# Kernel optimization log

Hardware: AMD Instinct MI355X
Metric: run time of the kernel (lower is better)

Reference implementation:

```python
import jax, jax.numpy as jnp
import numpy as np

NUM_STEPS = 20
START_IDX = 1


def setup_inputs() -> dict:
    key = jax.random.key(0)
    ks = jax.random.split(key, 14)
    B, L, D, H, E, K, V = 128, 49, 2048, 2048, 512, 512, 10000
    s = 0.02  # weight init scale to avoid saturating tanh/sigmoid
    return {
        "spatial": jax.random.normal(ks[0], (B, L, D), jnp.float32),
        "global_": jax.random.normal(ks[1], (B, D), jnp.float32),
        "embed": jax.random.normal(ks[2], (V, E), jnp.float32) * s,
        "W_ih": jax.random.normal(ks[3], (4 * H, E + D), jnp.float32) * s,
        "W_hh": jax.random.normal(ks[4], (4 * H, H), jnp.float32) * s,
        "b_ih": jnp.zeros((4 * H,), jnp.float32),
        "b_hh": jnp.zeros((4 * H,), jnp.float32),
        "W_v": jax.random.normal(ks[5], (D, K), jnp.float32) * s,
        "W_g": jax.random.normal(ks[6], (H, K), jnp.float32) * s,
        "w_h": jax.random.normal(ks[7], (K,), jnp.float32) * s,
        "W_p_w": jax.random.normal(ks[8], (V, H), jnp.float32) * s,
        "W_p_b": jnp.zeros((V,), jnp.float32),
        "W_init_h": jax.random.normal(ks[9], (D, H), jnp.float32) * s,
        "W_init_m": jax.random.normal(ks[10], (D, H), jnp.float32) * s,
    }


def reference(spatial, global_, embed, W_ih, W_hh, b_ih, b_hh,
              W_v, W_g, w_h, W_p_w, W_p_b, W_init_h, W_init_m):
    B = spatial.shape[0]
    Hdim = W_hh.shape[1]
    # initialize_state(features.global_)
    h0 = jnp.tanh(global_ @ W_init_h)
    m0 = jnp.tanh(global_ @ W_init_m)
    tok0 = jnp.full((B,), START_IDX, dtype=jnp.int32)
    # precompute attention projection of spatial features: [B, L, K]
    spatial_proj = jnp.einsum('bld,dk->blk', spatial, W_v)

    def step(carry, _):
        h, m, token = carry
        w = embed[token]                                  # [B, E]
        x = jnp.concatenate([w, global_], axis=1)         # [B, E+D]
        gates = x @ W_ih.T + b_ih + h @ W_hh.T + b_hh     # [B, 4H]
        i_g, f_g, g_g, o_g = jnp.split(gates, 4, axis=1)  # torch gate order
        m_new = jax.nn.sigmoid(f_g) * m + jax.nn.sigmoid(i_g) * jnp.tanh(g_g)
        h_new = jax.nn.sigmoid(o_g) * jnp.tanh(m_new)
        # spatial attention: z = w_h^T tanh(W_v V + W_g h)
        z = jnp.tanh(spatial_proj + (h_new @ W_g)[:, None, :]) @ w_h  # [B, L]
        alpha = jax.nn.softmax(z, axis=1)
        c = jnp.einsum('bl,bld->bd', alpha, spatial)      # [B, D]
        logits = (c + h_new) @ W_p_w.T + W_p_b            # [B, V]
        token_new = jnp.argmax(logits, axis=1).astype(jnp.int32)
        return (h_new, m_new, token_new), (logits, token_new)

    _, (logits_seq, tokens) = jax.lax.scan(step, (h0, m0, tok0), None, length=NUM_STEPS)
    # [T, B, V] -> [B, T, V]; [T, B] -> [B, T]
    return jnp.transpose(logits_seq, (1, 0, 2)), tokens.T
```

## Files before the change

kernel.cpp:

```cpp
#include <hip/hip_runtime.h>
#include <math.h>


typedef __attribute__((ext_vector_type(8))) short bf16x8;
typedef __attribute__((ext_vector_type(4))) float f32x4;

#define B_ 128
#define L_ 49
#define D_ 2048
#define H_ 2048
#define E_ 512
#define KA_ 512
#define V_ 10000
#define T_ 20
#define ED_ 2560
#define KT_ 4608
#define KT2_ 2560
#define H4_ 8192
#define VP_ 10112

__device__ __forceinline__ void split1(float x, short* hi, short* lo){
  unsigned u = __float_as_uint(x);
  *hi = (short)(u >> 16);
  float r = x - __uint_as_float(u & 0xffff0000u);
  *lo = (short)(__float_as_uint(r) >> 16);
}
__device__ __forceinline__ void split8(float4 a, float4 b, bf16x8& h, bf16x8& l){
  float xs[8] = {a.x,a.y,a.z,a.w,b.x,b.y,b.z,b.w};
#pragma unroll
  for (int i=0;i<8;++i){
    unsigned u = __float_as_uint(xs[i]);
    h[i] = (short)(u>>16);
    float r = xs[i] - __uint_as_float(u & 0xffff0000u);
    l[i] = (short)(__float_as_uint(r)>>16);
  }
}

#define MFMA16(d,a,b,c) d = __builtin_amdgcn_mfma_f32_16x16x32_bf16(a,b,c,0,0,0)

__device__ __forceinline__ void gl_lds16(const short* g, char* l){
  __builtin_amdgcn_global_load_lds(
      (const __attribute__((address_space(1))) unsigned int*)g,
      (__attribute__((address_space(3))) unsigned int*)l, 16, 0, 0);
}

__global__ __launch_bounds__(256)
void gemm_db(const short* __restrict__ A1h, const short* __restrict__ A1l, int lda1,
             const short* __restrict__ A2h, const short* __restrict__ A2l, int lda2,
             int ksplit,
             const short* __restrict__ Wh, const short* __restrict__ Wl, int ldw,
             float* __restrict__ Cp, int Mtot, int Np, int k_len)
{
  __shared__ __align__(16) char smem[131072];
  const int tid = threadIdx.x;
  const int wid = tid >> 6, lane = tid & 63;
  const int lr = lane & 15, lg = lane >> 4;
  const int m0 = blockIdx.z * 128;
  const int nblk = blockIdx.x * 128;
  const int kb0 = blockIdx.y * k_len;

  const int li8 = lane >> 3;
  const int kx  = 8 * ((lane & 7) ^ li8);

  f32x4 acc[8][2];
#pragma unroll
  for (int i=0;i<8;++i)
#pragma unroll
    for (int r=0;r<4;++r){ acc[i][0][r]=0.f; acc[i][1][r]=0.f; }

  const int rA = wid*32 + lr, rB = rA + 16;
  const int sw7 = lr & 7;

  auto STAGE = [&](int kb, int buf) {
    char* s = smem + buf*65536;
    if (wid == 0) {
#pragma unroll
      for (int j = 0; j < 16; ++j)
        gl_lds16(Wh + (long)(nblk + j*8 + li8)*ldw + kb + kx, s + j*1024);
    } else if (wid == 1) {
#pragma unroll
      for (int j = 0; j < 16; ++j)
        gl_lds16(Wl + (long)(nblk + j*8 + li8)*ldw + kb + kx, s + 16384 + j*1024);
    } else {
      const short *Ph, *Pl; int ldx, kc;
      if (kb < ksplit) { Ph = A1h; Pl = A1l; ldx = lda1; kc = kb; }
      else             { Ph = A2h; Pl = A2l; ldx = lda2; kc = kb - ksplit; }
      if (wid == 2) {
#pragma unroll
        for (int j = 0; j < 16; ++j)
          gl_lds16(Ph + (long)(m0 + j*8 + li8)*ldx + kc + kx, s + 32768 + j*1024);
      } else {
#pragma unroll
        for (int j = 0; j < 16; ++j)
          gl_lds16(Pl + (long)(m0 + j*8 + li8)*ldx + kc + kx, s + 49152 + j*1024);
      }
    }
  };

  auto COMPUTE = [&](int buf) {
    char* s = smem + buf*65536;
#pragma unroll
    for (int h = 0; h < 2; ++h) {
      const int c16 = (h<<2) + lg;
      const int swz = (c16 ^ sw7) << 4;
      const bf16x8 whA = *(const bf16x8*)(s +         rA*128 + swz);
      const bf16x8 wlA = *(const bf16x8*)(s + 16384 + rA*128 + swz);
      const bf16x8 whB = *(const bf16x8*)(s +         rB*128 + swz);
      const bf16x8 wlB = *(const bf16x8*)(s + 16384 + rB*128 + swz);
#pragma unroll
      for (int mt = 0; mt < 8; ++mt) {
        const int aoff = (mt*16 + lr)*128 + swz;
        const bf16x8 ah = *(const bf16x8*)(s + 32768 + aoff);
        const bf16x8 al = *(const bf16x8*)(s + 49152 + aoff);
        MFMA16(acc[mt][0], ah, whA, acc[mt][0]);
        MFMA16(acc[mt][1], ah, whB, acc[mt][1]);
        MFMA16(acc[mt][0], ah, wlA, acc[mt][0]);
        MFMA16(acc[mt][1], ah, wlB, acc[mt][1]);
        MFMA16(acc[mt][0], al, whA, acc[mt][0]);
        MFMA16(acc[mt][1], al, whB, acc[mt][1]);
      }
    }
  };

  STAGE(kb0, 0);
  asm volatile("s_waitcnt vmcnt(0)");
  __syncthreads();
  int cur = 0;
  for (int kt = 64; kt < k_len; kt += 64) {
    STAGE(kb0 + kt, cur ^ 1);
    COMPUTE(cur);
    asm volatile("s_waitcnt vmcnt(0)");
    __syncthreads();
    cur ^= 1;
  }
  COMPUTE(cur);

  const long srow = (long)blockIdx.y * Mtot + m0;
#pragma unroll
  for (int mt=0; mt<8; ++mt)
#pragma unroll
    for (int nt=0; nt<2; ++nt){
      const int col = nblk + wid*32 + nt*16 + lr;
#pragma unroll
      for (int r=0; r<4; ++r)
        Cp[(srow + mt*16 + 4*lg + r)*Np + col] = acc[mt][nt][r];
    }
}

__global__ __launch_bounds__(256)
void gemm_lds(const short* __restrict__ Ah, const short* __restrict__ Al, int lda,
              const short* __restrict__ Wh, const short* __restrict__ Wl, int ldw,
              float* __restrict__ Cp, int Mtot, int Np, int k_len)
{
  __shared__ __align__(16) char smem[65536];
  const int tid = threadIdx.x;
  const int wid = tid >> 6, lane = tid & 63;
  const int lr = lane & 15, lg = lane >> 4;
  const int m0 = blockIdx.z * 128;
  const int nblk = blockIdx.x * 128;
  const int kb0 = blockIdx.y * k_len;

  const int li8 = lane >> 3;
  const int kx  = 8 * ((lane & 7) ^ li8);

  f32x4 acc[8][2];
#pragma unroll
  for (int i=0;i<8;++i)
#pragma unroll
    for (int r=0;r<4;++r){ acc[i][0][r]=0.f; acc[i][1][r]=0.f; }

  const int rA = wid*32 + lr, rB = rA + 16;
  const int sw7 = lr & 7;

  for (int kt = 0; kt < k_len; kt += 64) {
    const int kb = kb0 + kt;
    if (wid == 0) {
#pragma unroll
      for (int j = 0; j < 16; ++j)
        gl_lds16(Wh + (long)(nblk + j*8 + li8)*ldw + kb + kx, smem + j*1024);
    } else if (wid == 1) {
#pragma unroll
      for (int j = 0; j < 16; ++j)
        gl_lds16(Wl + (long)(nblk + j*8 + li8)*ldw + kb + kx, smem + 16384 + j*1024);
    } else if (wid == 2) {
#pragma unroll
      for (int j = 0; j < 16; ++j)
        gl_lds16(Ah + (long)(m0 + j*8 + li8)*lda + kb + kx, smem + 32768 + j*1024);
    } else {
#pragma unroll
      for (int j = 0; j < 16; ++j)
        gl_lds16(Al + (long)(m0 + j*8 + li8)*lda + kb + kx, smem + 49152 + j*1024);
    }
    asm volatile("s_waitcnt vmcnt(0)");
    __syncthreads();

#pragma unroll
    for (int h = 0; h < 2; ++h) {
      const int c16 = (h<<2) + lg;
      const int swz = (c16 ^ sw7) << 4;
      const bf16x8 whA = *(const bf16x8*)(smem +         rA*128 + swz);
      const bf16x8 wlA = *(const bf16x8*)(smem + 16384 + rA*128 + swz);
      const bf16x8 whB = *(const bf16x8*)(smem +         rB*128 + swz);
      const bf16x8 wlB = *(const bf16x8*)(smem + 16384 + rB*128 + swz);
#pragma unroll
      for (int mt = 0; mt < 8; ++mt) {
        const int aoff = (mt*16 + lr)*128 + swz;
        const bf16x8 ah = *(const bf16x8*)(smem + 32768 + aoff);
        const bf16x8 al = *(const bf16x8*)(smem + 49152 + aoff);
        MFMA16(acc[mt][0], ah, whA, acc[mt][0]);
        MFMA16(acc[mt][1], ah, whB, acc[mt][1]);
        MFMA16(acc[mt][0], ah, wlA, acc[mt][0]);
        MFMA16(acc[mt][1], ah, wlB, acc[mt][1]);
        MFMA16(acc[mt][0], al, whA, acc[mt][0]);
        MFMA16(acc[mt][1], al, whB, acc[mt][1]);
      }
    }
    __syncthreads();
  }

  const long srow = (long)blockIdx.y * Mtot + m0;
#pragma unroll
  for (int mt=0; mt<8; ++mt)
#pragma unroll
    for (int nt=0; nt<2; ++nt){
      const int col = nblk + wid*32 + nt*16 + lr;
#pragma unroll
      for (int r=0; r<4; ++r)
        Cp[(srow + mt*16 + 4*lg + r)*Np + col] = acc[mt][nt][r];
    }
}

template<bool AF32>
__global__ __launch_bounds__(256)
void gemm_mfma(const void* Ahv, const void* Alv, int lda,
               const float* __restrict__ W1, int ldw1,
               const float* __restrict__ W2, int ldw2, int ksplit,
               float* __restrict__ Cp, int Mtot, int Np, int Nvalid, int k_len)
{
  const int tid = threadIdx.x;
  const int wid = tid >> 6, lane = tid & 63;
  const int lr = lane & 15, lg = lane >> 4;
  const int m0 = blockIdx.z * 128;
  const int nw = blockIdx.x * 128 + wid * 32;
  const int kb = blockIdx.y * k_len;

  int rowA = nw + lr;       if (rowA >= Nvalid) rowA = Nvalid - 1;
  int rowB = nw + 16 + lr;  if (rowB >= Nvalid) rowB = Nvalid - 1;

  f32x4 acc[8][2];
#pragma unroll
  for (int i=0;i<8;++i)
#pragma unroll
    for (int r=0;r<4;++r){ acc[i][0][r]=0.f; acc[i][1][r]=0.f; }

  for (int kk = 0; kk < k_len; kk += 32) {
    const int kg = kb + kk;
    const float *pA, *pB;
    if (W2 && kg >= ksplit) {
      pA = W2 + (long)rowA*ldw2 + (kg - ksplit) + 8*lg;
      pB = W2 + (long)rowB*ldw2 + (kg - ksplit) + 8*lg;
    } else {
      pA = W1 + (long)rowA*ldw1 + kg + 8*lg;
      pB = W1 + (long)rowB*ldw1 + kg + 8*lg;
    }
    bf16x8 whA, wlA, whB, wlB;
    split8(*(const float4*)pA, *(const float4*)(pA+4), whA, wlA);
    split8(*(const float4*)pB, *(const float4*)(pB+4), whB, wlB);

    bf16x8 ah[8], al[8];
    if constexpr (AF32) {
      const float* Af = (const float*)Ahv;
#pragma unroll
      for (int mt=0; mt<8; ++mt){
        const float* ap = Af + (long)(m0 + mt*16 + lr)*lda + kg + 8*lg;
        split8(*(const float4*)ap, *(const float4*)(ap+4), ah[mt], al[mt]);
      }
    } else {
      const short* Ah = (const short*)Ahv;
      const short* Al = (const short*)Alv;
#pragma unroll
      for (int mt=0; mt<8; ++mt){
        const long off = (long)(m0 + mt*16 + lr)*lda + kg + 8*lg;
        ah[mt] = *(const bf16x8*)(Ah + off);
        al[mt] = *(const bf16x8*)(Al + off);
      }
    }
#pragma unroll
    for (int mt=0; mt<8; ++mt){
      MFMA16(acc[mt][0], ah[mt], whA, acc[mt][0]);
      MFMA16(acc[mt][1], ah[mt], whB, acc[mt][1]);
      MFMA16(acc[mt][0], ah[mt], wlA, acc[mt][0]);
      MFMA16(acc[mt][1], ah[mt], wlB, acc[mt][1]);
      MFMA16(acc[mt][0], al[mt], whA, acc[mt][0]);
      MFMA16(acc[mt][1], al[mt], whB, acc[mt][1]);
    }
  }

  const long srow = (long)blockIdx.y * Mtot + m0;
#pragma unroll
  for (int mt=0; mt<8; ++mt)
#pragma unroll
// ... 218 lines not shown
    float e = (lane < L_) ? expf(v - mx) : 0.f;
    float sum = e;
#pragma unroll
    for (int off = 32; off > 0; off >>= 1) sum += __shfl_xor(sum, off);
    if (lane < L_) alph[lane] = e / sum;
  }
  __syncthreads();
  const int d4 = dh * 256 + tid;
  const float4* sp4 = (const float4*)spatial;
  float4 acc = ((const float4*)h)[(long)b * 512 + d4];
#pragma unroll 7
  for (int l = 0; l < L_; ++l) {
    const float w = alph[l];
    const float4 v = sp4[((long)b * L_ + l) * 512 + d4];
    acc.x = fmaf(w, v.x, acc.x); acc.y = fmaf(w, v.y, acc.y);
    acc.z = fmaf(w, v.z, acc.z); acc.w = fmaf(w, v.w, acc.w);
  }
  short4 hv, lv;
  split1(acc.x, &hv.x, &lv.x); split1(acc.y, &hv.y, &lv.y);
  split1(acc.z, &hv.z, &lv.z); split1(acc.w, &hv.w, &lv.w);
  *(short4*)&a_hi[(long)b * D_ + d4*4] = hv;
  *(short4*)&a_lo[(long)b * D_ + d4*4] = lv;
}

template<int SHG>
__global__ __launch_bounds__(256)
void attn_k(const float* __restrict__ sp_proj, const float* __restrict__ hgp,
            const float* __restrict__ w_h, const float* __restrict__ spatial,
            const float* __restrict__ h,
            short* __restrict__ a_hi, short* __restrict__ a_lo)
{
  const int b = blockIdx.x, half = blockIdx.y, tid = threadIdx.x;
  const int lane = tid & 63, wv = tid >> 6;
  __shared__ float hgs[KA_];
  __shared__ float whs[KA_];
  __shared__ float zs[L_];
  __shared__ float alph[L_];
  for (int i = tid; i < KA_; i += 256) {
    float s = 0.f;
#pragma unroll
    for (int sl = 0; sl < SHG; ++sl) s += hgp[((long)sl * B_ + b) * KA_ + i];
    hgs[i] = s; whs[i] = w_h[i];
  }
  __syncthreads();
  for (int l = wv; l < L_; l += 4) {
    const float* sp = sp_proj + ((long)b * L_ + l) * KA_;
    float s = 0.f;
    for (int k = lane; k < KA_; k += 64) s += whs[k] * tanhf(sp[k] + hgs[k]);
#pragma unroll
    for (int off = 32; off > 0; off >>= 1) s += __shfl_down(s, off);
    if (lane == 0) zs[l] = s;
  }
  __syncthreads();
  if (wv == 0) {
    float v = (lane < L_) ? zs[lane] : -INFINITY;
    float mx = v;
#pragma unroll
    for (int off = 32; off > 0; off >>= 1) mx = fmaxf(mx, __shfl_xor(mx, off));
    float e = (lane < L_) ? expf(v - mx) : 0.f;
    float sum = e;
#pragma unroll
    for (int off = 32; off > 0; off >>= 1) sum += __shfl_xor(sum, off);
    if (lane < L_) alph[lane] = e / sum;
  }
  __syncthreads();
  const int d4 = half * 256 + tid;
  const float4* h4 = (const float4*)h;
  const float4* sp4 = (const float4*)spatial;
  float4 acc = h4[(long)b * 512 + d4];
#pragma unroll 7
  for (int l = 0; l < L_; ++l) {
    const float w = alph[l];
    const float4 v = sp4[((long)b * L_ + l) * 512 + d4];
    acc.x = fmaf(w, v.x, acc.x); acc.y = fmaf(w, v.y, acc.y);
    acc.z = fmaf(w, v.z, acc.z); acc.w = fmaf(w, v.w, acc.w);
  }
  short4 hv, lv;
  split1(acc.x, &hv.x, &lv.x); split1(acc.y, &hv.y, &lv.y);
  split1(acc.z, &hv.z, &lv.z); split1(acc.w, &hv.w, &lv.w);
  *(short4*)&a_hi[(long)b * D_ + d4*4] = hv;
  *(short4*)&a_lo[(long)b * D_ + d4*4] = lv;
}

template<int S, bool GATHER>
__global__ __launch_bounds__(256)
void logits_argmax_k(const float* __restrict__ lp, const float* __restrict__ bias,
                     float* __restrict__ outL, int* __restrict__ tok,
                     float* __restrict__ tokout,
                     const float* __restrict__ embed,
                     short* __restrict__ xe_hi, short* __restrict__ xe_lo)
{
  const int b = blockIdx.x, tid = threadIdx.x;
  float bv = -INFINITY; int bi = 0x7fffffff;
  for (int j = tid; j < V_; j += 256) {
    float v = bias[j];
#pragma unroll
    for (int sl = 0; sl < S; ++sl) v += lp[((long)sl * B_ + b) * VP_ + j];
    outL[(long)b * (T_*V_) + j] = v;
    if (v > bv) { bv = v; bi = j; }
  }
  __shared__ float sv[256];
  __shared__ int   si[256];
  sv[tid] = bv; si[tid] = bi;
  __syncthreads();
  for (int s = 128; s > 0; s >>= 1) {
    if (tid < s) {
      const float ov = sv[tid + s]; const int oi = si[tid + s];
      if (ov > sv[tid] || (ov == sv[tid] && oi < si[tid])) { sv[tid] = ov; si[tid] = oi; }
    }
    __syncthreads();
  }
  if (tid == 0) { tok[b] = si[0]; tokout[(long)b * T_] = (float)si[0]; }
  if (GATHER) {
    __syncthreads();
    const int tk = si[0];
    const float* e = embed + (long)tk * E_;
    for (int i = tid; i < E_; i += 256)
      split1(e[i], &xe_hi[(long)b*E_ + i], &xe_lo[(long)b*E_ + i]);
  }
}

extern "C" void kernel_launch(void* const* d_in, const int* in_sizes, int n_in,
                              void* d_out, int out_size, void* d_ws, size_t ws_size,
                              hipStream_t stream)
{
  const float* spatial  = (const float*)d_in[0];
  const float* global_  = (const float*)d_in[1];
  const float* embed    = (const float*)d_in[2];
  const float* W_ih     = (const float*)d_in[3];
  const float* W_hh     = (const float*)d_in[4];
  const float* b_ih     = (const float*)d_in[5];
  const float* b_hh     = (const float*)d_in[6];
  const float* W_v      = (const float*)d_in[7];
  const float* W_g      = (const float*)d_in[8];
  const float* w_h      = (const float*)d_in[9];
  const float* W_p_w    = (const float*)d_in[10];
  const float* W_p_b    = (const float*)d_in[11];
  const float* W_init_h = (const float*)d_in[12];
  const float* W_init_m = (const float*)d_in[13];
  float* out = (float*)d_out;
  float* tokout = out + (long)B_ * T_ * V_;

  char* base = (char*)d_ws;
  const size_t NEED_PRE = 284983808;
  const size_t NEED_FB  = 62390784;
  if (ws_size < NEED_FB) return;

  if (ws_size >= NEED_PRE) {
    float* sp      = (float*)(base + 0);
    float* h       = (float*)(base + 12845056);
    float* m       = (float*)(base + 13893632);
    short* h_hi    = (short*)(base + 14942208);
    short* h_lo    = (short*)(base + 15466496);
    short* a_hi    = (short*)(base + 15990784);
    short* a_lo    = (short*)(base + 16515072);
    short* xe_hi   = (short*)(base + 17039360);
    short* xe_lo   = (short*)(base + 17170432);
    short* g_hi    = (short*)(base + 18350080);
    short* g_lo    = (short*)(base + 18874368);
    float* gconst  = (float*)(base + 19398656);
    int*   tok     = (int*)  (base + 23592960);
    float* arena   = (float*)(base + 23593472);
    short* Wcat_hi = (short*)(base + 107479552);
    short* Wcat_lo = (short*)(base + 149422592);
    short* Wp_hi   = (short*)(base + 191365632);
    short* Wp_lo   = (short*)(base + 232784384);
    short* WvT_hi  = (short*)(base + 274203136);
    short* WvT_lo  = (short*)(base + 276300288);
    short* WgT_hi  = (short*)(base + 278397440);
    short* WgT_lo  = (short*)(base + 280494592);
    float* zbuf    = (float*)(base + 282853888);

    init_tok_k<<<1, 128, 0, stream>>>(tok);
    split_plane_k<<<256, 256, 0, stream>>>(global_, (long)B_*D_, g_hi, g_lo);

    split_t_k<<<dim3(KA_/64, D_/64), 256, 0, stream>>>(W_v, D_, KA_, WvT_hi, WvT_lo);
    short* spA_hi = Wp_hi;
    short* spA_lo = (short*)((char*)Wp_hi + 25690112);
    split_plane_k<<<12544, 256, 0, stream>>>(spatial, (long)B_*L_*D_, spA_hi, spA_lo);
    float* sppart = (float*)Wcat_hi;
    gemm_db<<<dim3(4, 2, 49), 256, 0, stream>>>(
        spA_hi, spA_lo, D_, spA_hi, spA_lo, D_, 1<<30,
        WvT_hi, WvT_lo, D_, sppart, B_*L_, KA_, 1024);
    reduce_sp_k<2><<<3136, 256, 0, stream>>>((const float4*)sppart, (float4*)sp);

    short* Wglob_hi = Wp_hi;
    short* Wglob_lo = (short*)((char*)Wp_hi + 33554432);
    split_nt_k<<<dim3(2, H4_), 256, 0, stream>>>(W_ih + 512, ED_, H4_, D_, Wglob_hi, Wglob_lo, D_, 0);
    gemm_db<<<dim3(64, 4, 1), 256, 0, stream>>>(
        g_hi, g_lo, D_, g_hi, g_lo, D_, 1<<30,
        Wglob_hi, Wglob_lo, D_, arena, B_, H4_, 512);
    gred_k<4><<<(B_*H4_)/256, 256, 0, stream>>>(arena, b_ih, b_hh, gconst);

    split_nt_k<<<dim3(1, H4_), 256, 0, stream>>>(W_ih, ED_, H4_, E_, Wcat_hi, Wcat_lo, KT2_, 0);
    split_nt_k<<<dim3(2, H4_), 256, 0, stream>>>(W_hh, H_, H4_, H_, Wcat_hi, Wcat_lo, KT2_, E_);
    split_nt_k<<<dim3(2, VP_), 256, 0, stream>>>(W_p_w, H_, V_, H_, Wp_hi, Wp_lo, H_, 0);
    split_t_k<<<dim3(KA_/64, H_/64), 256, 0, stream>>>(W_g, H_, KA_, WgT_hi, WgT_lo);

    {
      short* WTh = (short*)arena;
      short* WTl = (short*)((char*)arena + 8388608);
      float* prt = (float*)((char*)arena + 16777216);
      split_t_k<<<dim3(H_/64, D_/64), 256, 0, stream>>>(W_init_h, D_, H_, WTh, WTl);
      gemm_lds<<<dim3(16, 16, 1), 256, 0, stream>>>(
          g_hi, g_lo, D_, WTh, WTl, D_, prt, B_, H_, 128);
      reduce_tanh_k<<<(B_*H_)/256, 256, 0, stream>>>(prt, 16, h, h_hi, h_lo);
      split_t_k<<<dim3(H_/64, D_/64), 256, 0, stream>>>(W_init_m, D_, H_, WTh, WTl);
      gemm_lds<<<dim3(16, 16, 1), 256, 0, stream>>>(
          g_hi, g_lo, D_, WTh, WTl, D_, prt, B_, H_, 128);
      reduce_tanh_k<<<(B_*H_)/256, 256, 0, stream>>>(prt, 16, m, nullptr, nullptr);
    }

    gather_emb_k<<<B_, 256, 0, stream>>>(embed, tok, xe_hi, xe_lo);

    for (int t = 0; t < T_; ++t) {
      gemm_db<<<dim3(64, 4, 1), 256, 0, stream>>>(
          xe_hi, xe_lo, E_, h_hi, h_lo, H_, E_,
          Wcat_hi, Wcat_lo, KT2_, arena, B_, H4_, 640);
      lstm_reduce_k<4><<<(B_*H_)/256, 256, 0, stream>>>(
          arena, gconst, nullptr, nullptr, h, m, h_hi, h_lo);
      gemm_lds<<<dim3(4, 32, 1), 256, 0, stream>>>(
          h_hi, h_lo, H_, WgT_hi, WgT_lo, H_, arena, B_, KA_, 64);
      hgz_k<<<B_, 256, 0, stream>>>(arena, sp, w_h, zbuf);
      cfull_k<<<dim3(B_, 2), 256, 0, stream>>>(zbuf, spatial, h, a_hi, a_lo);
      gemm_db<<<dim3(79, 4, 1), 256, 0, stream>>>(
          a_hi, a_lo, H_, a_hi, a_lo, H_, 1<<30,
          Wp_hi, Wp_lo, H_, arena, B_, VP_, 512);
      logits_argmax_k<4,true><<<B_, 256, 0, stream>>>(
          arena, W_p_b, out + (long)t * V_, tok, tokout + t,
          embed, xe_hi, xe_lo);
    }
  } else {
    float* sp    = (float*)(base + 0);
    float* WvTf  = (float*)(base + 12845056);
    float* WgTf  = (float*)(base + 17039360);
    float* h     = (float*)(base + 21233664);
    float* m     = (float*)(base + 22282240);
    short* h_hi  = (short*)(base + 24379392);
    short* h_lo  = (short*)(base + 24903680);
    short* a_hi  = (short*)(base + 25427968);
    short* a_lo  = (short*)(base + 25952256);
    short* xh_hi = (short*)(base + 26476544);
    short* xh_lo = (short*)(base + 27656192);
    int*   tok   = (int*)  (base + 28835840);
    float* arena = (float*)(base + 28836352);

    init_tok_k<<<1, 128, 0, stream>>>(tok);
    transpose_f32<<<dim3(KA_/64, D_/64), 256, 0, stream>>>(W_v, D_, KA_, WvTf);
    gemm_mfma<true><<<dim3(4, 1, 49), 256, 0, stream>>>(
        spatial, nullptr, D_, WvTf, D_, nullptr, 0, 1<<30, sp, B_*L_, KA_, KA_, D_);
    transpose_f32<<<dim3(KA_/64, H_/64), 256, 0, stream>>>(W_g, H_, KA_, WgTf);
    {
      float* WT  = arena;
      float* prt = (float*)((char*)arena + 16777216);
      transpose_f32<<<dim3(H_/64, D_/64), 256, 0, stream>>>(W_init_h, D_, H_, WT);
      gemm_mfma<true><<<dim3(16, 4, 1), 256, 0, stream>>>(
          global_, nullptr, D_, WT, D_, nullptr, 0, 1<<30, prt, B_, H_, H_, 512);
      reduce_tanh_k<<<(B_*H_)/256, 256, 0, stream>>>(prt, 4, h, h_hi, h_lo);
      transpose_f32<<<dim3(H_/64, D_/64), 256, 0, stream>>>(W_init_m, D_, H_, WT);
      gemm_mfma<true><<<dim3(16, 4, 1), 256, 0, stream>>>(
          global_, nullptr, D_, WT, D_, nullptr, 0, 1<<30, prt, B_, H_, H_, 512);
      reduce_tanh_k<<<(B_*H_)/256, 256, 0, stream>>>(prt, 4, m, nullptr, nullptr);
    }
    for (int t = 0; t < T_; ++t) {
      gather_xh_k<<<B_, 256, 0, stream>>>(embed, global_, h_hi, h_lo, tok, xh_hi, xh_lo);
      gemm_mfma<false><<<dim3(64, 8, 1), 256, 0, stream>>>(
          xh_hi, xh_lo, KT_, W_ih, ED_, W_hh, H_, ED_, arena, B_, H4_, H4_, 576);
      lstm_reduce_k<8><<<(B_*H_)/256, 256, 0, stream>>>(
          arena, nullptr, b_ih, b_hh, h, m, h_hi, h_lo);
      gemm_mfma<false><<<dim3(4, 16, 1), 256, 0, stream>>>(
          h_hi, h_lo, H_, WgTf, H_, nullptr, 0, 1<<30, arena, B_, KA_, KA_, 128);
      attn_k<16><<<dim3(B_, 2), 256, 0, stream>>>(sp, arena, w_h, spatial, h, a_hi, a_lo);
      gemm_mfma<false><<<dim3(79, 4, 1), 256, 0, stream>>>(
          a_hi, a_lo, H_, W_p_w, H_, nullptr, 0, 1<<30, arena, B_, VP_, V_, 512);
      logits_argmax_k<4,false><<<B_, 256, 0, stream>>>(
          arena, W_p_b, out + (long)t * V_, tok, tokout + t,
          nullptr, nullptr, nullptr);
    }
  }
}
```

Before: 2.762 ms.

## Unify GEMMs into one kernel staging one operand in LDS, other in registers

Replaces the two GEMM kernels with a templated kernel that double-buffers only one operand (weights or activations) in LDS while the other operand is loaded directly from global into registers. LDS use is halved so two blocks can fit per CU (launch_bounds 256,2), and split-K factors are doubled across the recurrent and setup GEMMs, with the partial-sum reduction kernels widened to match. This aims to raise occupancy and parallelism for the small-M LSTM-step GEMMs, at the cost of more register pressure, uncoalesced direct global loads, and more partial-sum traffic to reduce.

```diff
diff --git a/kernel.cpp b/kernel.cpp
--- a/kernel.cpp
+++ b/kernel.cpp
@@ -44,111 +44,11 @@
       (__attribute__((address_space(3))) unsigned int*)l, 16, 0, 0);
 }
 
-__global__ __launch_bounds__(256)
-void gemm_db(const short* __restrict__ A1h, const short* __restrict__ A1l, int lda1,
-             const short* __restrict__ A2h, const short* __restrict__ A2l, int lda2,
-             int ksplit,
-             const short* __restrict__ Wh, const short* __restrict__ Wl, int ldw,
-             float* __restrict__ Cp, int Mtot, int Np, int k_len)
-{
-  __shared__ __align__(16) char smem[131072];
-  const int tid = threadIdx.x;
-  const int wid = tid >> 6, lane = tid & 63;
-  const int lr = lane & 15, lg = lane >> 4;
-  const int m0 = blockIdx.z * 128;
-  const int nblk = blockIdx.x * 128;
-  const int kb0 = blockIdx.y * k_len;
-
-  const int li8 = lane >> 3;
-  const int kx  = 8 * ((lane & 7) ^ li8);
-
-  f32x4 acc[8][2];
-#pragma unroll
-  for (int i=0;i<8;++i)
-#pragma unroll
-    for (int r=0;r<4;++r){ acc[i][0][r]=0.f; acc[i][1][r]=0.f; }
-
-  const int rA = wid*32 + lr, rB = rA + 16;
-  const int sw7 = lr & 7;
-
-  auto STAGE = [&](int kb, int buf) {
-    char* s = smem + buf*65536;
-    if (wid == 0) {
-#pragma unroll
-      for (int j = 0; j < 16; ++j)
-        gl_lds16(Wh + (long)(nblk + j*8 + li8)*ldw + kb + kx, s + j*1024);
-    } else if (wid == 1) {
-#pragma unroll
-      for (int j = 0; j < 16; ++j)
-        gl_lds16(Wl + (long)(nblk + j*8 + li8)*ldw + kb + kx, s + 16384 + j*1024);
-    } else {
-      const short *Ph, *Pl; int ldx, kc;
-      if (kb < ksplit) { Ph = A1h; Pl = A1l; ldx = lda1; kc = kb; }
-      else             { Ph = A2h; Pl = A2l; ldx = lda2; kc = kb - ksplit; }
-      if (wid == 2) {
-#pragma unroll
-        for (int j = 0; j < 16; ++j)
-          gl_lds16(Ph + (long)(m0 + j*8 + li8)*ldx + kc + kx, s + 32768 + j*1024);
-      } else {
-#pragma unroll
-        for (int j = 0; j < 16; ++j)
-          gl_lds16(Pl + (long)(m0 + j*8 + li8)*ldx + kc + kx, s + 49152 + j*1024);
-      }
-    }
-  };
-
-  auto COMPUTE = [&](int buf) {
-    char* s = smem + buf*65536;
-#pragma unroll
-    for (int h = 0; h < 2; ++h) {
-      const int c16 = (h<<2) + lg;
-      const int swz = (c16 ^ sw7) << 4;
-      const bf16x8 whA = *(const bf16x8*)(s +         rA*128 + swz);
-      const bf16x8 wlA = *(const bf16x8*)(s + 16384 + rA*128 + swz);
-      const bf16x8 whB = *(const bf16x8*)(s +         rB*128 + swz);
-      const bf16x8 wlB = *(const bf16x8*)(s + 16384 + rB*128 + swz);
-#pragma unroll
-      for (int mt = 0; mt < 8; ++mt) {
-        const int aoff = (mt*16 + lr)*128 + swz;
-        const bf16x8 ah = *(const bf16x8*)(s + 32768 + aoff);
-        const bf16x8 al = *(const bf16x8*)(s + 49152 + aoff);
-        MFMA16(acc[mt][0], ah, whA, acc[mt][0]);
-        MFMA16(acc[mt][1], ah, whB, acc[mt][1]);
-        MFMA16(acc[mt][0], ah, wlA, acc[mt][0]);
-        MFMA16(acc[mt][1], ah, wlB, acc[mt][1]);
-        MFMA16(acc[mt][0], al, whA, acc[mt][0]);
-        MFMA16(acc[mt][1], al, whB, acc[mt][1]);
-      }
-    }
-  };
-
-  STAGE(kb0, 0);
-  asm volatile("s_waitcnt vmcnt(0)");
-  __syncthreads();
-  int cur = 0;
-  for (int kt = 64; kt < k_len; kt += 64) {
-    STAGE(kb0 + kt, cur ^ 1);
-    COMPUTE(cur);
-    asm volatile("s_waitcnt vmcnt(0)");
-    __syncthreads();
-    cur ^= 1;
-  }
-  COMPUTE(cur);
-
-  const long srow = (long)blockIdx.y * Mtot + m0;
-#pragma unroll
-  for (int mt=0; mt<8; ++mt)
-#pragma unroll
-    for (int nt=0; nt<2; ++nt){
-      const int col = nblk + wid*32 + nt*16 + lr;
-#pragma unroll
-      for (int r=0; r<4; ++r)
-        Cp[(srow + mt*16 + 4*lg + r)*Np + col] = acc[mt][nt][r];
-    }
-}
-
-__global__ __launch_bounds__(256)
-void gemm_lds(const short* __restrict__ Ah, const short* __restrict__ Al, int lda,
+template<bool STAGE_A>
+__global__ __launch_bounds__(256, 2)
+void gemm_v10(const short* __restrict__ A1h, const short* __restrict__ A1l, int lda1,
+              const short* __restrict__ A2h, const short* __restrict__ A2l, int lda2,
+              int ksplit,
               const short* __restrict__ Wh, const short* __restrict__ Wl, int ldw,
               float* __restrict__ Cp, int Mtot, int Np, int k_len)
 {
@@ -159,9 +59,10 @@
   const int m0 = blockIdx.z * 128;
   const int nblk = blockIdx.x * 128;
   const int kb0 = blockIdx.y * k_len;
-
   const int li8 = lane >> 3;
   const int kx  = 8 * ((lane & 7) ^ li8);
+  const int r0s = (wid & 1) * 64;
+  char* const splane = smem + (wid >> 1) * 16384;
 
   f32x4 acc[8][2];
 #pragma unroll
@@ -169,53 +70,110 @@
 #pragma unroll
     for (int r=0;r<4;++r){ acc[i][0][r]=0.f; acc[i][1][r]=0.f; }
 
-  const int rA = wid*32 + lr, rB = rA + 16;
+  const int rL = wid*32 + lr, rLB = rL + 16;
+  const long rWA = (long)(nblk + wid*32 + lr);
+  const long rWB = rWA + 16;
   const int sw7 = lr & 7;
 
+  auto STAGE = [&](int kb, int buf) {
+    char* s = splane + buf*32768;
+    if constexpr (STAGE_A) {
+      const short* P = (wid >= 2) ? A1l : A1h;
+#pragma unroll
+      for (int j = 0; j < 8; ++j)
+        gl_lds16(P + (long)(m0 + r0s + j*8 + li8)*lda1 + kb + kx, s + (r0s + j*8)*128);
+    } else {
+      const short* P = (wid >= 2) ? Wl : Wh;
+#pragma unroll
+      for (int j = 0; j < 8; ++j)
+        gl_lds16(P + (long)(nblk + r0s + j*8 + li8)*ldw + kb + kx, s + (r0s + j*8)*128);
+    }
+  };
+
+  STAGE(kb0, 0);
+  asm volatile("s_waitcnt vmcnt(0)");
+  __syncthreads();
+  int cur = 0;
+
   for (int kt = 0; kt < k_len; kt += 64) {
-    const int kb = kb0 + kt;
-    if (wid == 0) {
-#pragma unroll
-      for (int j = 0; j < 16; ++j)
-        gl_lds16(Wh + (long)(nblk + j*8 + li8)*ldw + kb + kx, smem + j*1024);
-    } else if (wid == 1) {
-#pragma unroll
-      for (int j = 0; j < 16; ++j)
-        gl_lds16(Wl + (long)(nblk + j*8 + li8)*ldw + kb + kx, smem + 16384 + j*1024);
-    } else if (wid == 2) {
-#pragma unroll
-      for (int j = 0; j < 16; ++j)
-        gl_lds16(Ah + (long)(m0 + j*8 + li8)*lda + kb + kx, smem + 32768 + j*1024);
+    const int kbb = kb0 + kt;
+    const bool last = (kt + 64 >= k_len);
+    char* s = smem + cur*32768;
+
+    if constexpr (STAGE_A) {
+      bf16x8 w0hA, w0lA, w0hB, w0lB, w1hA, w1lA, w1hB, w1lB;
+      {
+        const long c0 = kbb + 8*lg;
+        w0hA = *(const bf16x8*)(Wh + rWA*ldw + c0);
+        w0lA = *(const bf16x8*)(Wl + rWA*ldw + c0);
+        w0hB = *(const bf16x8*)(Wh + rWB*ldw + c0);
+        w0lB = *(const bf16x8*)(Wl + rWB*ldw + c0);
+        w1hA = *(const bf16x8*)(Wh + rWA*ldw + c0 + 32);
+        w1lA = *(const bf16x8*)(Wl + rWA*ldw + c0 + 32);
+        w1hB = *(const bf16x8*)(Wh + rWB*ldw + c0 + 32);
+        w1lB = *(const bf16x8*)(Wl + rWB*ldw + c0 + 32);
+      }
+      if (!last) STAGE(kbb + 64, cur ^ 1);
+#pragma unroll
+      for (int h = 0; h < 2; ++h) {
+        const int swz = ((h*4 + lg) ^ sw7) << 4;
+        const bf16x8 whA = h ? w1hA : w0hA;
+        const bf16x8 wlA = h ? w1lA : w0lA;
+        const bf16x8 whB = h ? w1hB : w0hB;
+        const bf16x8 wlB = h ? w1lB : w0lB;
+#pragma unroll
+        for (int mt = 0; mt < 8; ++mt) {
+          const int aoff = (mt*16 + lr)*128 + swz;
+          const bf16x8 ah = *(const bf16x8*)(s + aoff);
+          const bf16x8 al = *(const bf16x8*)(s + 16384 + aoff);
+          MFMA16(acc[mt][0], ah, whA, acc[mt][0]);
+          MFMA16(acc[mt][1], ah, whB, acc[mt][1]);
+          MFMA16(acc[mt][0], ah, wlA, acc[mt][0]);
+          MFMA16(acc[mt][1], ah, wlB, acc[mt][1]);
+          MFMA16(acc[mt][0], al, whA, acc[mt][0]);
+          MFMA16(acc[mt][1], al, whB, acc[mt][1]);
+        }
+      }
     } else {
-#pragma unroll
-      for (int j = 0; j < 16; ++j)
-        gl_lds16(Al + (long)(m0 + j*8 + li8)*lda + kb + kx, smem + 49152 + j*1024);
+      bf16x8 a0h[8], a0l[8], a1h[8], a1l[8];
+#pragma unroll
+      for (int h = 0; h < 2; ++h) {
+        const int kg = kbb + h*32;
+        const short *Ph, *Pl; long co; int ldx;
+        if (kg < ksplit) { Ph = A1h; Pl = A1l; co = kg; ldx = lda1; }
+        else             { Ph = A2h; Pl = A2l; co = kg - ksplit; ldx = lda2; }
+        co += 8*lg;
+#pragma unroll
+        for (int mt = 0; mt < 8; ++mt) {
+          const long o = (long)(m0 + mt*16 + lr)*ldx + co;
+          if (h == 0) { a0h[mt] = *(const bf16x8*)(Ph + o); a0l[mt] = *(const bf16x8*)(Pl + o); }
+          else        { a1h[mt] = *(const bf16x8*)(Ph + o); a1l[mt] = *(const bf16x8*)(Pl + o); }
+        }
+      }
+      if (!last) STAGE(kbb + 64, cur ^ 1);
+#pragma unroll
+      for (int h = 0; h < 2; ++h) {
+        const int swz = ((h*4 + lg) ^ sw7) << 4;
+        const bf16x8 whA = *(const bf16x8*)(s +         rL*128 + swz);
+        const bf16x8 wlA = *(const bf16x8*)(s + 16384 + rL*128 + swz);
+        const bf16x8 whB = *(const bf16x8*)(s +         rLB*128 + swz);
+        const bf16x8 wlB = *(const bf16x8*)(s + 16384 + rLB*128 + swz);
+#pragma unroll
+        for (int mt = 0; mt < 8; ++mt) {
+          const bf16x8 ah = h ? a1h[mt] : a0h[mt];
+          const bf16x8 al = h ? a1l[mt] : a0l[mt];
+          MFMA16(acc[mt][0], ah, whA, acc[mt][0]);
+          MFMA16(acc[mt][1], ah, whB, acc[mt][1]);
+          MFMA16(acc[mt][0], ah, wlA, acc[mt][0]);
+          MFMA16(acc[mt][1], ah, wlB, acc[mt][1]);
+          MFMA16(acc[mt][0], al, whA, acc[mt][0]);
+          MFMA16(acc[mt][1], al, whB, acc[mt][1]);
+        }
+      }
     }
     asm volatile("s_waitcnt vmcnt(0)");
     __syncthreads();
-
-#pragma unroll
-    for (int h = 0; h < 2; ++h) {
-      const int c16 = (h<<2) + lg;
-      const int swz = (c16 ^ sw7) << 4;
-      const bf16x8 whA = *(const bf16x8*)(smem +         rA*128 + swz);
-      const bf16x8 wlA = *(const bf16x8*)(smem + 16384 + rA*128 + swz);
-      const bf16x8 whB = *(const bf16x8*)(smem +         rB*128 + swz);
-      const bf16x8 wlB = *(const bf16x8*)(smem + 16384 + rB*128 + swz);
-#pragma unroll
-      for (int mt = 0; mt < 8; ++mt) {
-        const int aoff = (mt*16 + lr)*128 + swz;
-        const bf16x8 ah = *(const bf16x8*)(smem + 32768 + aoff);
-        const bf16x8 al = *(const bf16x8*)(smem + 49152 + aoff);
-        MFMA16(acc[mt][0], ah, whA, acc[mt][0]);
-        MFMA16(acc[mt][1], ah, whB, acc[mt][1]);
-        MFMA16(acc[mt][0], ah, wlA, acc[mt][0]);
-        MFMA16(acc[mt][1], ah, wlB, acc[mt][1]);
-        MFMA16(acc[mt][0], al, whA, acc[mt][0]);
-        MFMA16(acc[mt][1], al, whB, acc[mt][1]);
-      }
-    }
-    __syncthreads();
+    cur ^= 1;
   }
 
   const long srow = (long)blockIdx.y * Mtot + m0;
@@ -698,18 +656,18 @@
     short* spA_lo = (short*)((char*)Wp_hi + 25690112);
     split_plane_k<<<12544, 256, 0, stream>>>(spatial, (long)B_*L_*D_, spA_hi, spA_lo);
     float* sppart = (float*)Wcat_hi;
-    gemm_db<<<dim3(4, 2, 49), 256, 0, stream>>>(
+    gemm_v10<true><<<dim3(4, 4, 49), 256, 0, stream>>>(
         spA_hi, spA_lo, D_, spA_hi, spA_lo, D_, 1<<30,
-        WvT_hi, WvT_lo, D_, sppart, B_*L_, KA_, 1024);
-    reduce_sp_k<2><<<3136, 256, 0, stream>>>((const float4*)sppart, (float4*)sp);
+        WvT_hi, WvT_lo, D_, sppart, B_*L_, KA_, 512);
+    reduce_sp_k<4><<<3136, 256, 0, stream>>>((const float4*)sppart, (float4*)sp);
 
     short* Wglob_hi = Wp_hi;
     short* Wglob_lo = (short*)((char*)Wp_hi + 33554432);
     split_nt_k<<<dim3(2, H4_), 256, 0, stream>>>(W_ih + 512, ED_, H4_, D_, Wglob_hi, Wglob_lo, D_, 0);
-    gemm_db<<<dim3(64, 4, 1), 256, 0, stream>>>(
+    gemm_v10<false><<<dim3(64, 8, 1), 256, 0, stream>>>(
         g_hi, g_lo, D_, g_hi, g_lo, D_, 1<<30,
-        Wglob_hi, Wglob_lo, D_, arena, B_, H4_, 512);
-    gred_k<4><<<(B_*H4_)/256, 256, 0, stream>>>(arena, b_ih, b_hh, gconst);
+        Wglob_hi, Wglob_lo, D_, arena, B_, H4_, 256);
+    gred_k<8><<<(B_*H4_)/256, 256, 0, stream>>>(arena, b_ih, b_hh, gconst);
 
     split_nt_k<<<dim3(1, H4_), 256, 0, stream>>>(W_ih, ED_, H4_, E_, Wcat_hi, Wcat_lo, KT2_, 0);
     split_nt_k<<<dim3(2, H4_), 256, 0, stream>>>(W_hh, H_, H4_, H_, Wcat_hi, Wcat_lo, KT2_, E_);
@@ -721,31 +679,34 @@
       short* WTl = (short*)((char*)arena + 8388608);
       float* prt = (float*)((char*)arena + 16777216);
       split_t_k<<<dim3(H_/64, D_/64), 256, 0, stream>>>(W_init_h, D_, H_, WTh, WTl);
-      gemm_lds<<<dim3(16, 16, 1), 256, 0, stream>>>(
-          g_hi, g_lo, D_, WTh, WTl, D_, prt, B_, H_, 128);
+      gemm_v10<false><<<dim3(16, 16, 1), 256, 0, stream>>>(
+          g_hi, g_lo, D_, g_hi, g_lo, D_, 1<<30,
+          WTh, WTl, D_, prt, B_, H_, 128);
       reduce_tanh_k<<<(B_*H_)/256, 256, 0, stream>>>(prt, 16, h, h_hi, h_lo);
       split_t_k<<<dim3(H_/64, D_/64), 256, 0, stream>>>(W_init_m, D_, H_, WTh, WTl);
-      gemm_lds<<<dim3(16, 16, 1), 256, 0, stream>>>(
-          g_hi, g_lo, D_, WTh, WTl, D_, prt, B_, H_, 128);
+      gemm_v10<false><<<dim3(16, 16, 1), 256, 0, stream>>>(
+          g_hi, g_lo, D_, g_hi, g_lo, D_, 1<<30,
+          WTh, WTl, D_, prt, B_, H_, 128);
       reduce_tanh_k<<<(B_*H_)/256, 256, 0, stream>>>(prt, 16, m, nullptr, nullptr);
     }
 
     gather_emb_k<<<B_, 256, 0, stream>>>(embed, tok, xe_hi, xe_lo);
 
     for (int t = 0; t < T_; ++t) {
-      gemm_db<<<dim3(64, 4, 1), 256, 0, stream>>>(
+      gemm_v10<false><<<dim3(64, 8, 1), 256, 0, stream>>>(
           xe_hi, xe_lo, E_, h_hi, h_lo, H_, E_,
-          Wcat_hi, Wcat_lo, KT2_, arena, B_, H4_, 640);
-      lstm_reduce_k<4><<<(B_*H_)/256, 256, 0, stream>>>(
+          Wcat_hi, Wcat_lo, KT2_, arena, B_, H4_, 320);
+      lstm_reduce_k<8><<<(B_*H_)/256, 256, 0, stream>>>(
           arena, gconst, nullptr, nullptr, h, m, h_hi, h_lo);
-      gemm_lds<<<dim3(4, 32, 1), 256, 0, stream>>>(
-          h_hi, h_lo, H_, WgT_hi, WgT_lo, H_, arena, B_, KA_, 64);
+      gemm_v10<false><<<dim3(4, 32, 1), 256, 0, stream>>>(
+          h_hi, h_lo, H_, h_hi, h_lo, H_, 1<<30,
+          WgT_hi, WgT_lo, H_, arena, B_, KA_, 64);
       hgz_k<<<B_, 256, 0, stream>>>(arena, sp, w_h, zbuf);
       cfull_k<<<dim3(B_, 2), 256, 0, stream>>>(zbuf, spatial, h, a_hi, a_lo);
-      gemm_db<<<dim3(79, 4, 1), 256, 0, stream>>>(
+      gemm_v10<false><<<dim3(79, 8, 1), 256, 0, stream>>>(
           a_hi, a_lo, H_, a_hi, a_lo, H_, 1<<30,
-          Wp_hi, Wp_lo, H_, arena, B_, VP_, 512);
-      logits_argmax_k<4,true><<<B_, 256, 0, stream>>>(
+          Wp_hi, Wp_lo, H_, arena, B_, VP_, 256);
+      logits_argmax_k<8,true><<<B_, 256, 0, stream>>>(
           arena, W_p_b, out + (long)t * V_, tok, tokout + t,
           embed, xe_hi, xe_lo);
     }
```

New measurement: 4.441 ms. 1.61x slower.

## Swap double-buffered GEMMs for wider split-K LDS GEMM and split logits argmax

Applied to the files above, without the earlier changes.

The per-step LSTM-gate and vocabulary-projection GEMMs move from the double-buffered gemm_db kernel to a single-buffered gemm_lds kernel, which gains support for two A operands. The split-K factor doubles from 4 to 8, giving twice as many workgroups and halving each block's K range. The logits reduce plus argmax is split into a vocab-partitioned kernel across 8 blocks per row and a small finalize kernel that also gathers the next embedding. The aim is more parallelism for these small-batch GEMMs and the reduction, at the cost of more partial-sum traffic, an extra launch per step, and losing load/compute overlap.

```diff
diff --git a/kernel.cpp b/kernel.cpp
--- a/kernel.cpp
+++ b/kernel.cpp
@@ -45,6 +45,96 @@
 }
 
 __global__ __launch_bounds__(256)
+void gemm_lds(const short* __restrict__ A1h, const short* __restrict__ A1l, int lda1,
+              const short* __restrict__ A2h, const short* __restrict__ A2l, int lda2,
+              int ksplit,
+              const short* __restrict__ Wh, const short* __restrict__ Wl, int ldw,
+              float* __restrict__ Cp, int Mtot, int Np, int k_len)
+{
+  __shared__ __align__(16) char smem[65536];
+  const int tid = threadIdx.x;
+  const int wid = tid >> 6, lane = tid & 63;
+  const int lr = lane & 15, lg = lane >> 4;
+  const int m0 = blockIdx.z * 128;
+  const int nblk = blockIdx.x * 128;
+  const int kb0 = blockIdx.y * k_len;
+
+  const int li8 = lane >> 3;
+  const int kx  = 8 * ((lane & 7) ^ li8);
+
+  f32x4 acc[8][2];
+#pragma unroll
+  for (int i=0;i<8;++i)
+#pragma unroll
+    for (int r=0;r<4;++r){ acc[i][0][r]=0.f; acc[i][1][r]=0.f; }
+
+  const int rA = wid*32 + lr, rB = rA + 16;
+  const int sw7 = lr & 7;
+
+  for (int kt = 0; kt < k_len; kt += 64) {
+    const int kb = kb0 + kt;
+    if (wid == 0) {
+#pragma unroll
+      for (int j = 0; j < 16; ++j)
+        gl_lds16(Wh + (long)(nblk + j*8 + li8)*ldw + kb + kx, smem + j*1024);
+    } else if (wid == 1) {
+#pragma unroll
+      for (int j = 0; j < 16; ++j)
+        gl_lds16(Wl + (long)(nblk + j*8 + li8)*ldw + kb + kx, smem + 16384 + j*1024);
+    } else {
+      const short *Ph, *Pl; int ldx, kc;
+      if (kb < ksplit) { Ph = A1h; Pl = A1l; ldx = lda1; kc = kb; }
+      else             { Ph = A2h; Pl = A2l; ldx = lda2; kc = kb - ksplit; }
+      if (wid == 2) {
+#pragma unroll
+        for (int j = 0; j < 16; ++j)
+          gl_lds16(Ph + (long)(m0 + j*8 + li8)*ldx + kc + kx, smem + 32768 + j*1024);
+      } else {
+#pragma unroll
+        for (int j = 0; j < 16; ++j)
+          gl_lds16(Pl + (long)(m0 + j*8 + li8)*ldx + kc + kx, smem + 49152 + j*1024);
+      }
+    }
+    asm volatile("s_waitcnt vmcnt(0)");
+    __syncthreads();
+
+#pragma unroll
+    for (int h = 0; h < 2; ++h) {
+      const int c16 = (h<<2) + lg;
+      const int swz = (c16 ^ sw7) << 4;
+      const bf16x8 whA = *(const bf16x8*)(smem +         rA*128 + swz);
+      const bf16x8 wlA = *(const bf16x8*)(smem + 16384 + rA*128 + swz);
+      const bf16x8 whB = *(const bf16x8*)(smem +         rB*128 + swz);
+      const bf16x8 wlB = *(const bf16x8*)(smem + 16384 + rB*128 + swz);
+#pragma unroll
+      for (int mt = 0; mt < 8; ++mt) {
+        const int aoff = (mt*16 + lr)*128 + swz;
+        const bf16x8 ah = *(const bf16x8*)(smem + 32768 + aoff);
+        const bf16x8 al = *(const bf16x8*)(smem + 49152 + aoff);
+        MFMA16(acc[mt][0], ah, whA, acc[mt][0]);
+        MFMA16(acc[mt][1], ah, whB, acc[mt][1]);
+        MFMA16(acc[mt][0], ah, wlA, acc[mt][0]);
+        MFMA16(acc[mt][1], ah, wlB, acc[mt][1]);
+        MFMA16(acc[mt][0], al, whA, acc[mt][0]);
+        MFMA16(acc[mt][1], al, whB, acc[mt][1]);
+      }
+    }
+    __syncthreads();
+  }
+
+  const long srow = (long)blockIdx.y * Mtot + m0;
+#pragma unroll
+  for (int mt=0; mt<8; ++mt)
+#pragma unroll
+    for (int nt=0; nt<2; ++nt){
+      const int col = nblk + wid*32 + nt*16 + lr;
+#pragma unroll
+      for (int r=0; r<4; ++r)
+        Cp[(srow + mt*16 + 4*lg + r)*Np + col] = acc[mt][nt][r];
+    }
+}
+
+__global__ __launch_bounds__(256)
 void gemm_db(const short* __restrict__ A1h, const short* __restrict__ A1l, int lda1,
              const short* __restrict__ A2h, const short* __restrict__ A2l, int lda2,
              int ksplit,
@@ -134,89 +224,6 @@
     cur ^= 1;
   }
   COMPUTE(cur);
-
-  const long srow = (long)blockIdx.y * Mtot + m0;
-#pragma unroll
-  for (int mt=0; mt<8; ++mt)
-#pragma unroll
-    for (int nt=0; nt<2; ++nt){
-      const int col = nblk + wid*32 + nt*16 + lr;
-#pragma unroll
-      for (int r=0; r<4; ++r)
-        Cp[(srow + mt*16 + 4*lg + r)*Np + col] = acc[mt][nt][r];
-    }
-}
-
-__global__ __launch_bounds__(256)
-void gemm_lds(const short* __restrict__ Ah, const short* __restrict__ Al, int lda,
-              const short* __restrict__ Wh, const short* __restrict__ Wl, int ldw,
-              float* __restrict__ Cp, int Mtot, int Np, int k_len)
-{
-  __shared__ __align__(16) char smem[65536];
-  const int tid = threadIdx.x;
-  const int wid = tid >> 6, lane = tid & 63;
-  const int lr = lane & 15, lg = lane >> 4;
-  const int m0 = blockIdx.z * 128;
-  const int nblk = blockIdx.x * 128;
-  const int kb0 = blockIdx.y * k_len;
-
-  const int li8 = lane >> 3;
-  const int kx  = 8 * ((lane & 7) ^ li8);
-
-  f32x4 acc[8][2];
-#pragma unroll
-  for (int i=0;i<8;++i)
-#pragma unroll
-    for (int r=0;r<4;++r){ acc[i][0][r]=0.f; acc[i][1][r]=0.f; }
-
-  const int rA = wid*32 + lr, rB = rA + 16;
-  const int sw7 = lr & 7;
-
-  for (int kt = 0; kt < k_len; kt += 64) {
-    const int kb = kb0 + kt;
-    if (wid == 0) {
-#pragma unroll
-      for (int j = 0; j < 16; ++j)
-        gl_lds16(Wh + (long)(nblk + j*8 + li8)*ldw + kb + kx, smem + j*1024);
-    } else if (wid == 1) {
-#pragma unroll
-      for (int j = 0; j < 16; ++j)
-        gl_lds16(Wl + (long)(nblk + j*8 + li8)*ldw + kb + kx, smem + 16384 + j*1024);
-    } else if (wid == 2) {
-#pragma unroll
-      for (int j = 0; j < 16; ++j)
-        gl_lds16(Ah + (long)(m0 + j*8 + li8)*lda + kb + kx, smem + 32768 + j*1024);
-    } else {
-#pragma unroll
-      for (int j = 0; j < 16; ++j)
-        gl_lds16(Al + (long)(m0 + j*8 + li8)*lda + kb + kx, smem + 49152 + j*1024);
-    }
-    asm volatile("s_waitcnt vmcnt(0)");
-    __syncthreads();
-
-#pragma unroll
-    for (int h = 0; h < 2; ++h) {
-      const int c16 = (h<<2) + lg;
-      const int swz = (c16 ^ sw7) << 4;
-      const bf16x8 whA = *(const bf16x8*)(smem +         rA*128 + swz);
-      const bf16x8 wlA = *(const bf16x8*)(smem + 16384 + rA*128 + swz);
-      const bf16x8 whB = *(const bf16x8*)(smem +         rB*128 + swz);
-      const bf16x8 wlB = *(const bf16x8*)(smem + 16384 + rB*128 + swz);
-#pragma unroll
-      for (int mt = 0; mt < 8; ++mt) {
-        const int aoff = (mt*16 + lr)*128 + swz;
-        const bf16x8 ah = *(const bf16x8*)(smem + 32768 + aoff);
-        const bf16x8 al = *(const bf16x8*)(smem + 49152 + aoff);
-        MFMA16(acc[mt][0], ah, whA, acc[mt][0]);
-        MFMA16(acc[mt][1], ah, whB, acc[mt][1]);
-        MFMA16(acc[mt][0], ah, wlA, acc[mt][0]);
-        MFMA16(acc[mt][1], ah, wlB, acc[mt][1]);
-        MFMA16(acc[mt][0], al, whA, acc[mt][0]);
-        MFMA16(acc[mt][1], al, whB, acc[mt][1]);
-      }
-    }
-    __syncthreads();
-  }
 
   const long srow = (long)blockIdx.y * Mtot + m0;
 #pragma unroll
@@ -601,13 +608,66 @@
   *(short4*)&a_lo[(long)b * D_ + d4*4] = lv;
 }
 
-template<int S, bool GATHER>
+template<int S>
+__global__ __launch_bounds__(256)
+void logits_part_k(const float* __restrict__ lp, const float* __restrict__ bias,
+                   float* __restrict__ outL, float* __restrict__ cval,
+                   int* __restrict__ cidx)
+{
+  const int b = blockIdx.x, s8 = blockIdx.y, tid = threadIdx.x;
+  const int j0 = s8 * 1264;
+  float bv = -INFINITY; int bi = 0x7fffffff;
+  for (int j = j0 + tid; j < j0 + 1264; j += 256) {
+    if (j < V_) {
+      float v = bias[j];
+#pragma unroll
+      for (int sl = 0; sl < S; ++sl) v += lp[((long)sl * B_ + b) * VP_ + j];
+      outL[(long)b * (T_*V_) + j] = v;
+      if (v > bv) { bv = v; bi = j; }
+    }
+  }
+  __shared__ float sv[256];
+  __shared__ int   si[256];
+  sv[tid] = bv; si[tid] = bi;
+  __syncthreads();
+  for (int s = 128; s > 0; s >>= 1) {
+    if (tid < s) {
+      const float ov = sv[tid + s]; const int oi = si[tid + s];
+      if (ov > sv[tid] || (ov == sv[tid] && oi < si[tid])) { sv[tid] = ov; si[tid] = oi; }
+    }
+    __syncthreads();
+  }
+  if (tid == 0) { cval[b*8 + s8] = sv[0]; cidx[b*8 + s8] = si[0]; }
+}
+
+__global__ __launch_bounds__(256)
+void argmax_fin_k(const float* __restrict__ cval, const int* __restrict__ cidx,
+                  int* __restrict__ tok, float* __restrict__ tokout,
+                  const float* __restrict__ embed,
+                  short* __restrict__ xe_hi, short* __restrict__ xe_lo)
+{
+  const int b = blockIdx.x, tid = threadIdx.x;
+  __shared__ int stk;
+  if (tid == 0) {
+    float bv = cval[b*8]; int bi = cidx[b*8];
+#pragma unroll
+    for (int s = 1; s < 8; ++s) {
+      const float v = cval[b*8 + s]; const int i = cidx[b*8 + s];
+      if (v > bv || (v == bv && i < bi)) { bv = v; bi = i; }
+    }
+    tok[b] = bi; tokout[(long)b * T_] = (float)bi; stk = bi;
+  }
+  __syncthreads();
+  const float* e = embed + (long)stk * E_;
+  for (int i = tid; i < E_; i += 256)
+    split1(e[i], &xe_hi[(long)b*E_ + i], &xe_lo[(long)b*E_ + i]);
+}
+
+template<int S>
 __global__ __launch_bounds__(256)
 void logits_argmax_k(const float* __restrict__ lp, const float* __restrict__ bias,
                      float* __restrict__ outL, int* __restrict__ tok,
-                     float* __restrict__ tokout,
-                     const float* __restrict__ embed,
-                     short* __restrict__ xe_hi, short* __restrict__ xe_lo)
+                     float* __restrict__ tokout)
 {
   const int b = blockIdx.x, tid = threadIdx.x;
   float bv = -INFINITY; int bi = 0x7fffffff;
@@ -630,13 +690,6 @@
     __syncthreads();
   }
   if (tid == 0) { tok[b] = si[0]; tokout[(long)b * T_] = (float)si[0]; }
-  if (GATHER) {
-    __syncthreads();
-    const int tk = si[0];
-    const float* e = embed + (long)tk * E_;
-    for (int i = tid; i < E_; i += 256)
-      split1(e[i], &xe_hi[(long)b*E_ + i], &xe_lo[(long)b*E_ + i]);
-  }
 }
 
 extern "C" void kernel_launch(void* const* d_in, const int* in_sizes, int n_in,
@@ -689,6 +742,8 @@
     short* WgT_hi  = (short*)(base + 278397440);
     short* WgT_lo  = (short*)(base + 280494592);
     float* zbuf    = (float*)(base + 282853888);
+    float* cval    = (float*)(base + 282886656);
+    int*   cidx    = (int*)  (base + 282890752);
 
     init_tok_k<<<1, 128, 0, stream>>>(tok);
     split_plane_k<<<256, 256, 0, stream>>>(global_, (long)B_*D_, g_hi, g_lo);
@@ -722,32 +777,36 @@
       float* prt = (float*)((char*)arena + 16777216);
       split_t_k<<<dim3(H_/64, D_/64), 256, 0, stream>>>(W_init_h, D_, H_, WTh, WTl);
       gemm_lds<<<dim3(16, 16, 1), 256, 0, stream>>>(
-          g_hi, g_lo, D_, WTh, WTl, D_, prt, B_, H_, 128);
+          g_hi, g_lo, D_, g_hi, g_lo, D_, 1<<30,
+          WTh, WTl, D_, prt, B_, H_, 128);
       reduce_tanh_k<<<(B_*H_)/256, 256, 0, stream>>>(prt, 16, h, h_hi, h_lo);
       split_t_k<<<dim3(H_/64, D_/64), 256, 0, stream>>>(W_init_m, D_, H_, WTh, WTl);
       gemm_lds<<<dim3(16, 16, 1), 256, 0, stream>>>(
-          g_hi, g_lo, D_, WTh, WTl, D_, prt, B_, H_, 128);
+          g_hi, g_lo, D_, g_hi, g_lo, D_, 1<<30,
+          WTh, WTl, D_, prt, B_, H_, 128);
       reduce_tanh_k<<<(B_*H_)/256, 256, 0, stream>>>(prt, 16, m, nullptr, nullptr);
     }
 
     gather_emb_k<<<B_, 256, 0, stream>>>(embed, tok, xe_hi, xe_lo);
 
     for (int t = 0; t < T_; ++t) {
-      gemm_db<<<dim3(64, 4, 1), 256, 0, stream>>>(
+      gemm_lds<<<dim3(64, 8, 1), 256, 0, stream>>>(
           xe_hi, xe_lo, E_, h_hi, h_lo, H_, E_,
-          Wcat_hi, Wcat_lo, KT2_, arena, B_, H4_, 640);
-      lstm_reduce_k<4><<<(B_*H_)/256, 256, 0, stream>>>(
+          Wcat_hi, Wcat_lo, KT2_, arena, B_, H4_, 320);
+      lstm_reduce_k<8><<<(B_*H_)/256, 256, 0, stream>>>(
           arena, gconst, nullptr, nullptr, h, m, h_hi, h_lo);
       gemm_lds<<<dim3(4, 32, 1), 256, 0, stream>>>(
-          h_hi, h_lo, H_, WgT_hi, WgT_lo, H_, arena, B_, KA_, 64);
+          h_hi, h_lo, H_, h_hi, h_lo, H_, 1<<30,
+          WgT_hi, WgT_lo, H_, arena, B_, KA_, 64);
       hgz_k<<<B_, 256, 0, stream>>>(arena, sp, w_h, zbuf);
       cfull_k<<<dim3(B_, 2), 256, 0, stream>>>(zbuf, spatial, h, a_hi, a_lo);
-      gemm_db<<<dim3(79, 4, 1), 256, 0, stream>>>(
+      gemm_lds<<<dim3(79, 8, 1), 256, 0, stream>>>(
           a_hi, a_lo, H_, a_hi, a_lo, H_, 1<<30,
-          Wp_hi, Wp_lo, H_, arena, B_, VP_, 512);
-      logits_argmax_k<4,true><<<B_, 256, 0, stream>>>(
-          arena, W_p_b, out + (long)t * V_, tok, tokout + t,
-          embed, xe_hi, xe_lo);
+          Wp_hi, Wp_lo, H_, arena, B_, VP_, 256);
+      logits_part_k<8><<<dim3(B_, 8), 256, 0, stream>>>(
+          arena, W_p_b, out + (long)t * V_, cval, cidx);
+      argmax_fin_k<<<B_, 256, 0, stream>>>(
+          cval, cidx, tok, tokout + t, embed, xe_hi, xe_lo);
     }
   } else {
     float* sp    = (float*)(base + 0);
@@ -792,9 +851,8 @@
       attn_k<16><<<dim3(B_, 2), 256, 0, stream>>>(sp, arena, w_h, spatial, h, a_hi, a_lo);
       gemm_mfma<false><<<dim3(79, 4, 1), 256, 0, stream>>>(
           a_hi, a_lo, H_, W_p_w, H_, nullptr, 0, 1<<30, arena, B_, VP_, V_, 512);
-      logits_argmax_k<4,false><<<B_, 256, 0, stream>>>(
-          arena, W_p_b, out + (long)t * V_, tok, tokout + t,
-          nullptr, nullptr, nullptr);
-    }
-  }
-}
+      logits_argmax_k<4><<<B_, 256, 0, stream>>>(
+          arena, W_p_b, out + (long)t * V_, tok, tokout + t);
+    }
+  }
+}
```

Measured after the change: 2.660 ms. 3.7% less time.
